# Performance work log

Hardware: AMD Instinct MI355X
Metric: run time of the kernel (lower is better)

Reference implementation:

```python
import jax, jax.numpy as jnp
import numpy as np

B, L, F, P = 128, 256, 4, 4   # dialogs, dialog length, future/past links
IN, H, C = 1024, 256, 7
N = B * L


def _build_edges():
    # same structure as build_intra_graph: self-loop + F future + P past per node
    i = np.arange(L)
    ss, tt = [], []
    for d in range(-P, F + 1):
        j = i + d
        m = (j >= 0) & (j < L)
        ss.append(i[m]); tt.append(j[m])
    s = np.concatenate(ss); t = np.concatenate(tt)
    offs = (np.arange(B) * L)[:, None]
    S = (s[None, :] + offs).ravel()
    T = (t[None, :] + offs).ravel()
    return np.stack([S, T]).astype(np.int32)


def setup_inputs() -> dict:
    key = jax.random.key(0)
    ks = jax.random.split(key, 16)
    ei = _build_edges()
    speakers = np.asarray(jax.random.randint(ks[0], (N,), 0, 2), dtype=np.int32)
    rel = (speakers[ei[0]] * speakers[ei[1]]).astype(np.int32)
    sd_in = 1.0 / np.sqrt(IN)
    sd_h = 1.0 / np.sqrt(H)
    return {
        "input": jax.random.normal(ks[1], (N, IN), jnp.float32),
        "dialog_lengths": jnp.full((B,), L, jnp.int32),
        "speakers": jnp.asarray(speakers),
        "labels": jax.random.randint(ks[2], (N,), 0, C, jnp.int32),
        "edge_index": jnp.asarray(ei),
        "rel_type": jnp.asarray(rel),
        # RGCNConv(IN, H, num_relations=2): per-relation weight, root weight, bias
        "W_rgcn": jax.random.normal(ks[3], (2, IN, H), jnp.float32) * sd_in,
        "W_root": jax.random.normal(ks[4], (IN, H), jnp.float32) * sd_in,
        "b_rgcn": jax.random.normal(ks[5], (H,), jnp.float32) * 0.01,
        # GraphConv(H, H): lin_rel (on aggregated neighbors, with bias), lin_root (no bias)
        "W_rel": jax.random.normal(ks[6], (H, H), jnp.float32) * sd_h,
        "b_rel": jax.random.normal(ks[7], (H,), jnp.float32) * 0.01,
        "W_grt": jax.random.normal(ks[8], (H, H), jnp.float32) * sd_h,
        # skip_con: Linear(IN, H)
        "W_skip": jax.random.normal(ks[9], (IN, H), jnp.float32) * sd_in,
        "b_skip": jax.random.normal(ks[10], (H,), jnp.float32) * 0.01,
        # classify: Linear(H, C)
        "W_cls": jax.random.normal(ks[11], (H, C), jnp.float32) * sd_h,
        "b_cls": jax.random.normal(ks[12], (C,), jnp.float32) * 0.01,
    }


def reference(input, dialog_lengths, speakers, labels, edge_index, rel_type,
              W_rgcn, W_root, b_rgcn, W_rel, b_rel, W_grt,
              W_skip, b_skip, W_cls, b_cls):
    n = input.shape[0]
    src, dst = edge_index[0], edge_index[1]
    seg = jax.ops.segment_sum

    # --- RGCNConv: out_i = x_i @ W_root + b + sum_r mean_{j in N_r(i)} x_j @ W_r
    t = jnp.einsum('ni,rio->rno', input, W_rgcn)      # [2, N, H]
    msg = t[rel_type, src]                            # [E, H] relation-specific messages
    h = input @ W_root + b_rgcn
    for r in range(2):
        m = (rel_type == r).astype(input.dtype)       # [E]
        s = seg(msg * m[:, None], dst, num_segments=n)
        cnt = seg(m, dst, num_segments=n)
        h = h + s / jnp.maximum(cnt, 1.0)[:, None]    # mean aggregation per relation

    # --- GraphConv (aggr='add'): out_i = W_rel @ sum_j h_j + b_rel + W_grt @ h_i
    neigh = seg(h[src], dst, num_segments=n)          # [N, H]
    h2 = neigh @ W_rel + b_rel + h @ W_grt

    # --- skip connection + classifier
    out = (h2 + input @ W_skip + b_skip) @ W_cls + b_cls  # [N, C]

    # --- cross entropy (mean)
    logp = jax.nn.log_softmax(out, axis=-1)
    loss = -jnp.mean(jnp.take_along_axis(logp, labels[:, None].astype(jnp.int32), axis=1))
    return out, loss
```

## Files before the change

kernel.cpp:

```cpp
#include <hip/hip_runtime.h>

#define NN 32768
#define INF 1024
#define HF 256

typedef __bf16 bf16x8 __attribute__((ext_vector_type(8)));
typedef float f32x4 __attribute__((ext_vector_type(4)));

__device__ __forceinline__ float bf2f(unsigned short u) {
  union { unsigned int i; float f; } v; v.i = ((unsigned int)u) << 16; return v.f;
}
__device__ __forceinline__ unsigned short f2bf(float f) {
  union { float f; unsigned int i; } v; v.f = f;
  unsigned int x = v.i;
  return (unsigned short)((x + 0x7fffu + ((x >> 16) & 1u)) >> 16);
}

__device__ __forceinline__ void ld_lds16(const unsigned short* g, unsigned short* l) {
  __builtin_amdgcn_global_load_lds(
      (__attribute__((address_space(1))) const unsigned int*)g,
      (__attribute__((address_space(3))) unsigned int*)l, 16, 0, 0);
}

__global__ __launch_bounds__(256)
void diagcn_prep(const float* __restrict__ x, const float* __restrict__ Wrgcn,
                 const float* __restrict__ Wroot, const float* __restrict__ Wskip,
                 const float* __restrict__ Wgrt, const float* __restrict__ Wrel,
                 unsigned short* __restrict__ Xbf, unsigned short* __restrict__ WbigT,
                 unsigned short* __restrict__ WsmT) {
  int bid = blockIdx.x;
  if (bid < 32768) {
    int idx = bid * 256 + threadIdx.x;
    float4 v = ((const float4*)x)[idx];
    ushort4 u; u.x = f2bf(v.x); u.y = f2bf(v.y); u.z = f2bf(v.z); u.w = f2bf(v.w);
    ((ushort4*)Xbf)[idx] = u;
    return;
  }
  __shared__ float tile[64 * 65];
  int tb = bid - 32768;
  const float* src;
  int k0, ncol0;
  unsigned short* dst;
  int ldd, nrow0;
  if (tb < 256) {
    int tn = tb >> 4, tk = tb & 15;
    int mat = tn >> 2;
    src = (mat == 0) ? Wrgcn : (mat == 1) ? (Wrgcn + 262144) : (mat == 2) ? Wroot : Wskip;
    k0 = tk * 64; ncol0 = (tn & 3) * 64;
    dst = WbigT; ldd = 1024; nrow0 = tn * 64;
  } else {
    int t2 = tb - 256;
    int tn = t2 >> 3, tk = t2 & 7;
    src = (tk < 4) ? Wgrt : Wrel;
    k0 = (tk & 3) * 64; ncol0 = tn * 64;
    dst = WsmT; ldd = 512; nrow0 = tn * 64;
    k0 = k0;
  }
  int kdst0 = (tb < 256) ? k0 : (((tb - 256) & 7) * 64);
  int c = threadIdx.x & 63, rb = threadIdx.x >> 6;
#pragma unroll
  for (int it = 0; it < 16; ++it) {
    int r = rb + it * 4;
    tile[r * 65 + c] = src[(size_t)(k0 + r) * 256 + ncol0 + c];
  }
  __syncthreads();
  int kk = threadIdx.x & 63;
#pragma unroll
  for (int it = 0; it < 16; ++it) {
    int nn = rb + it * 4;
    dst[(size_t)(nrow0 + nn) * ldd + kdst0 + kk] = f2bf(tile[kk * 65 + nn]);
  }
}

template <int EPI, int NT, int L2NT>
__global__ __launch_bounds__(256)
void diagcn_gemm(const unsigned short* __restrict__ A, const unsigned short* __restrict__ BT,
                 void* __restrict__ Cout, const unsigned short* __restrict__ Yfull,
                 const float* __restrict__ brel, const float* __restrict__ bskip, int K) {
  __shared__ unsigned short As[128 * 64];
  __shared__ unsigned short Bs[128 * 64];
  const int tid = threadIdx.x;
  const int w = tid >> 6, lane = tid & 63;
  const int wm = w >> 1, wn = w & 1;
  const int quad = lane >> 4, l15 = lane & 15;
  const int b = blockIdx.x;
  const int m0 = (((b & 7) << 5) + (b >> (3 + L2NT))) << 7;
  const int n0 = ((b >> 3) & (NT - 1)) << 7;
  const int rowg = lane >> 3;
  const int kbsw = (lane & 7) ^ rowg;

  f32x4 acc[4][4] = {};

  const unsigned short* Abase = A + (size_t)m0 * K + kbsw * 8;
  const unsigned short* Bbase = BT + (size_t)n0 * K + kbsw * 8;

  for (int k0 = 0; k0 < K; k0 += 64) {
#pragma unroll
    for (int t = 0; t < 4; ++t) {
      int grp = w * 4 + t;
      int rl = grp * 8 + rowg;
      ld_lds16(Abase + (size_t)rl * K + k0, &As[grp * 512]);
      ld_lds16(Bbase + (size_t)rl * K + k0, &Bs[grp * 512]);
    }
    __syncthreads();
#pragma unroll
    for (int ks = 0; ks < 2; ++ks) {
      bf16x8 av[4], bv[4];
      int kb = ks * 4 + quad;
#pragma unroll
      for (int i = 0; i < 4; ++i) {
        int ra = wm * 64 + i * 16 + l15;
        int rb = wn * 64 + i * 16 + l15;
        av[i] = *(const bf16x8*)&As[ra * 64 + ((kb ^ (ra & 7)) << 3)];
        bv[i] = *(const bf16x8*)&Bs[rb * 64 + ((kb ^ (rb & 7)) << 3)];
      }
#pragma unroll
      for (int i = 0; i < 4; ++i)
#pragma unroll
        for (int j = 0; j < 4; ++j)
          acc[i][j] = __builtin_amdgcn_mfma_f32_16x16x32_bf16(av[i], bv[j], acc[i][j], 0, 0, 0);
    }
    __syncthreads();
  }

  if (EPI == 0) {
    unsigned short* Y = (unsigned short*)Cout;
#pragma unroll
    for (int i = 0; i < 4; ++i)
#pragma unroll
      for (int j = 0; j < 4; ++j) {
        int row = m0 + wm * 64 + i * 16 + quad * 4;
        int col = n0 + wn * 64 + j * 16 + l15;
#pragma unroll
        for (int r = 0; r < 4; ++r)
          Y[(size_t)(row + r) * 1024 + col] = f2bf(acc[i][j][r]);
      }
  } else {
    float* Z = (float*)Cout;
#pragma unroll
    for (int i = 0; i < 4; ++i)
#pragma unroll
      for (int j = 0; j < 4; ++j) {
        int row = m0 + wm * 64 + i * 16 + quad * 4;
        int col = n0 + wn * 64 + j * 16 + l15;
#pragma unroll
        for (int r = 0; r < 4; ++r) {
          float v = acc[i][j][r] + brel[col] + bskip[col] +
                    bf2f(Yfull[(size_t)(row + r) * 1024 + 768 + col]);
          Z[(size_t)(row + r) * 256 + col] = v;
        }
      }
  }
}

__global__ __launch_bounds__(256)
void diagcn_h(const unsigned short* __restrict__ Y, const int* __restrict__ spk,
              const float* __restrict__ brgcn, unsigned short* __restrict__ A2) {
  int b = blockIdx.x;
  int node = ((b & 7) << 12) + ((b >> 3) << 2) + (threadIdx.x >> 6);
  int lane = threadIdx.x & 63, c0 = lane << 2;
  int p = node & 255, dbase = node - p;
  int si = spk[node];
  float a0[4] = {0, 0, 0, 0}, a1[4] = {0, 0, 0, 0};
  float n0 = 0.f, n1 = 0.f;
#pragma unroll
  for (int d = -4; d <= 4; ++d) {
    int pj = p + d;
    float w = (pj >= 0 && pj < 256) ? 1.f : 0.f;
    int jc = pj < 0 ? 0 : (pj > 255 ? 255 : pj);
    int nj = dbase + jc;
    int rel = si & spk[nj];
    ushort4 v = *(const ushort4*)&Y[(size_t)nj * 1024 + (rel << 8) + c0];
    float w1 = rel ? w : 0.f, w0 = rel ? 0.f : w;
    a0[0] += bf2f(v.x) * w0; a1[0] += bf2f(v.x) * w1;
    a0[1] += bf2f(v.y) * w0; a1[1] += bf2f(v.y) * w1;
    a0[2] += bf2f(v.z) * w0; a1[2] += bf2f(v.z) * w1;
    a0[3] += bf2f(v.w) * w0; a1[3] += bf2f(v.w) * w1;
    n0 += w0; n1 += w1;
  }
  ushort4 vr = *(const ushort4*)&Y[(size_t)node * 1024 + 512 + c0];
  float4 bb = *(const float4*)&brgcn[c0];
  float i0 = 1.f / fmaxf(n0, 1.f), i1 = 1.f / fmaxf(n1, 1.f);
  ushort4 u;
  u.x = f2bf(bf2f(vr.x) + bb.x + a0[0] * i0 + a1[0] * i1);
  u.y = f2bf(bf2f(vr.y) + bb.y + a0[1] * i0 + a1[1] * i1);
  u.z = f2bf(bf2f(vr.z) + bb.z + a0[2] * i0 + a1[2] * i1);
  u.w = f2bf(bf2f(vr.w) + bb.w + a0[3] * i0 + a1[3] * i1);
  *(ushort4*)&A2[(size_t)node * 512 + c0] = u;
}

__global__ __launch_bounds__(256)
void diagcn_neigh(unsigned short* __restrict__ A2) {
  int b = blockIdx.x;
  int node = ((b & 7) << 12) + ((b >> 3) << 2) + (threadIdx.x >> 6);
  int lane = threadIdx.x & 63, c0 = lane << 2;
  int p = node & 255, dbase = node - p;
  float s[4] = {0, 0, 0, 0};
#pragma unroll
  for (int d = -4; d <= 4; ++d) {
    int pj = p + d;
    float w = (pj >= 0 && pj < 256) ? 1.f : 0.f;
    int jc = pj < 0 ? 0 : (pj > 255 ? 255 : pj);
    ushort4 v = *(const ushort4*)&A2[(size_t)(dbase + jc) * 512 + c0];
    s[0] += bf2f(v.x) * w; s[1] += bf2f(v.y) * w;
    s[2] += bf2f(v.z) * w; s[3] += bf2f(v.w) * w;
  }
  ushort4 u; u.x = f2bf(s[0]); u.y = f2bf(s[1]); u.z = f2bf(s[2]); u.w = f2bf(s[3]);
  *(ushort4*)&A2[(size_t)node * 512 + 256 + c0] = u;
}

__global__ __launch_bounds__(256)
void diagcn_out(const float* __restrict__ z, const float* __restrict__ Wcls,
                const float* __restrict__ bcls, const int* __restrict__ labels,
                float* __restrict__ out, float* __restrict__ lossp) {
  __shared__ float Wc[256 * 7 + 7];
  for (int i = threadIdx.x; i < 256 * 7 + 7; i += 256)
    Wc[i] = (i < 1792) ? Wcls[i] : bcls[i - 1792];
  __syncthreads();
  int node = blockIdx.x * 4 + (threadIdx.x >> 6);
  int lane = threadIdx.x & 63;
  int c0 = lane << 2;
  float4 zv = *(const float4*)&z[(size_t)node * 256 + c0];
  float zz[4] = {zv.x, zv.y, zv.z, zv.w};
  float pr[7] = {0, 0, 0, 0, 0, 0, 0};
#pragma unroll
  for (int cc = 0; cc < 4; ++cc) {
    const float* wr = &Wc[(c0 + cc) * 7];
#pragma unroll
    for (int k = 0; k < 7; ++k) pr[k] += zz[cc] * wr[k];
  }
#pragma unroll
  for (int o = 32; o > 0; o >>= 1)
#pragma unroll
    for (int k = 0; k < 7; ++k) pr[k] += __shfl_down(pr[k], o, 64);
  if (lane == 0) {
    float o7[7], m = -1e30f;
#pragma unroll
    for (int k = 0; k < 7; ++k) {
      o7[k] = pr[k] + Wc[1792 + k];
      out[(size_t)node * 7 + k] = o7[k];
      m = fmaxf(m, o7[k]);
    }
    float s = 0;
#pragma unroll
    for (int k = 0; k < 7; ++k) s += expf(o7[k] - m);
    int lab = labels[node];
    lossp[node] = m + logf(s) - o7[lab];
  }
}

__global__ void diagcn_lred(const float* __restrict__ lp, float* __restrict__ dst) {
  __shared__ float sm[256];
  float s = 0;
  for (int i = threadIdx.x; i < NN; i += 256) s += lp[i];
  sm[threadIdx.x] = s;
  __syncthreads();
  for (int o = 128; o > 0; o >>= 1) {
    if (threadIdx.x < o) sm[threadIdx.x] += sm[threadIdx.x + o];
    __syncthreads();
  }
  if (threadIdx.x == 0) dst[0] = sm[0] * (1.0f / (float)NN);
}

extern "C" void kernel_launch(void* const* d_in, const int* in_sizes, int n_in,
                              void* d_out, int out_size, void* d_ws, size_t ws_size,
                              hipStream_t stream) {
  const float* x      = (const float*)d_in[0];
  const int* speakers = (const int*)d_in[2];
  const int* labels   = (const int*)d_in[3];
  const float* Wrgcn  = (const float*)d_in[6];
  const float* Wroot  = (const float*)d_in[7];
  const float* brgcn  = (const float*)d_in[8];
  const float* Wrel   = (const float*)d_in[9];
  const float* brel   = (const float*)d_in[10];
  const float* Wgrt   = (const float*)d_in[11];
  const float* Wskip  = (const float*)d_in[12];
  const float* bskip  = (const float*)d_in[13];
  const float* Wcls   = (const float*)d_in[14];
  const float* bcls   = (const float*)d_in[15];
  float* out = (float*)d_out;

  const size_t OFF_XBF  = 0;
  const size_t OFF_WBIG = 67108864;
  const size_t OFF_WSM  = 69206016;
  const size_t OFF_Y    = 69468160;
  const size_t OFF_A2   = 136577024;
  const size_t NEED     = 170131456;
  if (ws_size < NEED) return;

  char* ws = (char*)d_ws;
  unsigned short* Xbf   = (unsigned short*)(ws + OFF_XBF);
  unsigned short* WbigT = (unsigned short*)(ws + OFF_WBIG);
  unsigned short* WsmT  = (unsigned short*)(ws + OFF_WSM);
  unsigned short* Y     = (unsigned short*)(ws + OFF_Y);
  unsigned short* A2    = (unsigned short*)(ws + OFF_A2);
  float* z              = (float*)(ws + OFF_XBF);
  float* lossp          = (float*)(ws + OFF_XBF + 33554432);

  diagcn_prep<<<dim3(32768 + 288), dim3(256), 0, stream>>>(x, Wrgcn, Wroot, Wskip, Wgrt, Wrel,
                                                           Xbf, WbigT, WsmT);
  diagcn_gemm<0, 8, 3><<<dim3(2048), dim3(256), 0, stream>>>(Xbf, WbigT, (void*)Y,
                                                             nullptr, nullptr, nullptr, 1024);
  diagcn_h<<<dim3(NN / 4), dim3(256), 0, stream>>>(Y, speakers, brgcn, A2);
  diagcn_neigh<<<dim3(NN / 4), dim3(256), 0, stream>>>(A2);
  diagcn_gemm<1, 2, 1><<<dim3(512), dim3(256), 0, stream>>>(A2, WsmT, (void*)z,
                                                            Y, brel, bskip, 512);
  diagcn_out<<<dim3(NN / 4), dim3(256), 0, stream>>>(z, Wcls, bcls, labels, out, lossp);
  diagcn_lred<<<dim3(1), dim3(256), 0, stream>>>(lossp, out + (size_t)NN * 7);
}
```

Before: 405.1 us.

## Fuse classifier and loss into second GEMM epilogue, widen gather vectors

The second GEMM now covers all 256 output columns per block (64-row tiles), so each row's full hidden vector is in registers. The epilogue applies the biases, the skip term and the 7-class classifier, then reduces log-softmax cross-entropy via shuffles and atomics into the loss. This removes the fp32 z round-trip and the separate output and loss-reduction kernels. The aggregation kernels also switch to 8-wide bf16 loads, two nodes per wave. Costs are an atomic-order-dependent loss and a larger per-block B tile in LDS.

```diff
diff --git a/kernel.cpp b/kernel.cpp
--- a/kernel.cpp
+++ b/kernel.cpp
@@ -6,6 +6,7 @@
 
 typedef __bf16 bf16x8 __attribute__((ext_vector_type(8)));
 typedef float f32x4 __attribute__((ext_vector_type(4)));
+typedef unsigned short u16x8 __attribute__((ext_vector_type(8)));
 
 __device__ __forceinline__ float bf2f(unsigned short u) {
   union { unsigned int i; float f; } v; v.i = ((unsigned int)u) << 16; return v.f;
@@ -27,9 +28,10 @@
                  const float* __restrict__ Wroot, const float* __restrict__ Wskip,
                  const float* __restrict__ Wgrt, const float* __restrict__ Wrel,
                  unsigned short* __restrict__ Xbf, unsigned short* __restrict__ WbigT,
-                 unsigned short* __restrict__ WsmT) {
+                 unsigned short* __restrict__ WsmT, float* __restrict__ loss) {
   int bid = blockIdx.x;
   if (bid < 32768) {
+    if (bid == 0 && threadIdx.x == 0) loss[0] = 0.f;
     int idx = bid * 256 + threadIdx.x;
     float4 v = ((const float4*)x)[idx];
     ushort4 u; u.x = f2bf(v.x); u.y = f2bf(v.y); u.z = f2bf(v.z); u.w = f2bf(v.w);
@@ -54,7 +56,6 @@
     src = (tk < 4) ? Wgrt : Wrel;
     k0 = (tk & 3) * 64; ncol0 = tn * 64;
     dst = WsmT; ldd = 512; nrow0 = tn * 64;
-    k0 = k0;
   }
   int kdst0 = (tb < 256) ? k0 : (((tb - 256) & 7) * 64);
   int c = threadIdx.x & 63, rb = threadIdx.x >> 6;
@@ -72,11 +73,10 @@
   }
 }
 
-template <int EPI, int NT, int L2NT>
-__global__ __launch_bounds__(256)
-void diagcn_gemm(const unsigned short* __restrict__ A, const unsigned short* __restrict__ BT,
-                 void* __restrict__ Cout, const unsigned short* __restrict__ Yfull,
-                 const float* __restrict__ brel, const float* __restrict__ bskip, int K) {
+__global__ __launch_bounds__(256)
+void diagcn_gemm1(const unsigned short* __restrict__ A, const unsigned short* __restrict__ BT,
+                  unsigned short* __restrict__ Y) {
+  const int K = 1024;
   __shared__ unsigned short As[128 * 64];
   __shared__ unsigned short Bs[128 * 64];
   const int tid = threadIdx.x;
@@ -84,13 +84,12 @@
   const int wm = w >> 1, wn = w & 1;
   const int quad = lane >> 4, l15 = lane & 15;
   const int b = blockIdx.x;
-  const int m0 = (((b & 7) << 5) + (b >> (3 + L2NT))) << 7;
-  const int n0 = ((b >> 3) & (NT - 1)) << 7;
+  const int m0 = (((b & 7) << 5) + (b >> 6)) << 7;
+  const int n0 = ((b >> 3) & 7) << 7;
   const int rowg = lane >> 3;
   const int kbsw = (lane & 7) ^ rowg;
 
   f32x4 acc[4][4] = {};
-
   const unsigned short* Abase = A + (size_t)m0 * K + kbsw * 8;
   const unsigned short* Bbase = BT + (size_t)n0 * K + kbsw * 8;
 
@@ -110,9 +109,9 @@
 #pragma unroll
       for (int i = 0; i < 4; ++i) {
         int ra = wm * 64 + i * 16 + l15;
-        int rb = wn * 64 + i * 16 + l15;
+        int rb2 = wn * 64 + i * 16 + l15;
         av[i] = *(const bf16x8*)&As[ra * 64 + ((kb ^ (ra & 7)) << 3)];
-        bv[i] = *(const bf16x8*)&Bs[rb * 64 + ((kb ^ (rb & 7)) << 3)];
+        bv[i] = *(const bf16x8*)&Bs[rb2 * 64 + ((kb ^ (rb2 & 7)) << 3)];
       }
 #pragma unroll
       for (int i = 0; i < 4; ++i)
@@ -122,46 +121,28 @@
     }
     __syncthreads();
   }
-
-  if (EPI == 0) {
-    unsigned short* Y = (unsigned short*)Cout;
-#pragma unroll
-    for (int i = 0; i < 4; ++i)
-#pragma unroll
-      for (int j = 0; j < 4; ++j) {
-        int row = m0 + wm * 64 + i * 16 + quad * 4;
-        int col = n0 + wn * 64 + j * 16 + l15;
-#pragma unroll
-        for (int r = 0; r < 4; ++r)
-          Y[(size_t)(row + r) * 1024 + col] = f2bf(acc[i][j][r]);
-      }
-  } else {
-    float* Z = (float*)Cout;
-#pragma unroll
-    for (int i = 0; i < 4; ++i)
-#pragma unroll
-      for (int j = 0; j < 4; ++j) {
-        int row = m0 + wm * 64 + i * 16 + quad * 4;
-        int col = n0 + wn * 64 + j * 16 + l15;
-#pragma unroll
-        for (int r = 0; r < 4; ++r) {
-          float v = acc[i][j][r] + brel[col] + bskip[col] +
-                    bf2f(Yfull[(size_t)(row + r) * 1024 + 768 + col]);
-          Z[(size_t)(row + r) * 256 + col] = v;
-        }
-      }
-  }
+#pragma unroll
+  for (int i = 0; i < 4; ++i)
+#pragma unroll
+    for (int j = 0; j < 4; ++j) {
+      int row = m0 + wm * 64 + i * 16 + quad * 4;
+      int col = n0 + wn * 64 + j * 16 + l15;
+#pragma unroll
+      for (int r = 0; r < 4; ++r)
+        Y[(size_t)(row + r) * 1024 + col] = f2bf(acc[i][j][r]);
+    }
 }
 
 __global__ __launch_bounds__(256)
 void diagcn_h(const unsigned short* __restrict__ Y, const int* __restrict__ spk,
               const float* __restrict__ brgcn, unsigned short* __restrict__ A2) {
   int b = blockIdx.x;
-  int node = ((b & 7) << 12) + ((b >> 3) << 2) + (threadIdx.x >> 6);
-  int lane = threadIdx.x & 63, c0 = lane << 2;
+  int wv = threadIdx.x >> 6, lane = threadIdx.x & 63;
+  int half = lane >> 5, li = lane & 31, c0 = li << 3;
+  int node = ((b & 7) << 12) + ((b >> 3) << 3) + wv * 2 + half;
   int p = node & 255, dbase = node - p;
   int si = spk[node];
-  float a0[4] = {0, 0, 0, 0}, a1[4] = {0, 0, 0, 0};
+  float a0[8] = {}, a1[8] = {};
   float n0 = 0.f, n1 = 0.f;
 #pragma unroll
   for (int d = -4; d <= 4; ++d) {
@@ -170,96 +151,145 @@
     int jc = pj < 0 ? 0 : (pj > 255 ? 255 : pj);
     int nj = dbase + jc;
     int rel = si & spk[nj];
-    ushort4 v = *(const ushort4*)&Y[(size_t)nj * 1024 + (rel << 8) + c0];
+    u16x8 v = *(const u16x8*)&Y[(size_t)nj * 1024 + (rel << 8) + c0];
     float w1 = rel ? w : 0.f, w0 = rel ? 0.f : w;
-    a0[0] += bf2f(v.x) * w0; a1[0] += bf2f(v.x) * w1;
-    a0[1] += bf2f(v.y) * w0; a1[1] += bf2f(v.y) * w1;
-    a0[2] += bf2f(v.z) * w0; a1[2] += bf2f(v.z) * w1;
-    a0[3] += bf2f(v.w) * w0; a1[3] += bf2f(v.w) * w1;
+#pragma unroll
+    for (int k = 0; k < 8; ++k) {
+      float f = bf2f(v[k]);
+      a0[k] += f * w0; a1[k] += f * w1;
+    }
     n0 += w0; n1 += w1;
   }
-  ushort4 vr = *(const ushort4*)&Y[(size_t)node * 1024 + 512 + c0];
-  float4 bb = *(const float4*)&brgcn[c0];
+  u16x8 vr = *(const u16x8*)&Y[(size_t)node * 1024 + 512 + c0];
   float i0 = 1.f / fmaxf(n0, 1.f), i1 = 1.f / fmaxf(n1, 1.f);
-  ushort4 u;
-  u.x = f2bf(bf2f(vr.x) + bb.x + a0[0] * i0 + a1[0] * i1);
-  u.y = f2bf(bf2f(vr.y) + bb.y + a0[1] * i0 + a1[1] * i1);
-  u.z = f2bf(bf2f(vr.z) + bb.z + a0[2] * i0 + a1[2] * i1);
-  u.w = f2bf(bf2f(vr.w) + bb.w + a0[3] * i0 + a1[3] * i1);
-  *(ushort4*)&A2[(size_t)node * 512 + c0] = u;
+  u16x8 u;
+#pragma unroll
+  for (int k = 0; k < 8; ++k)
+    u[k] = f2bf(bf2f(vr[k]) + brgcn[c0 + k] + a0[k] * i0 + a1[k] * i1);
+  *(u16x8*)&A2[(size_t)node * 512 + c0] = u;
 }
 
 __global__ __launch_bounds__(256)
 void diagcn_neigh(unsigned short* __restrict__ A2) {
   int b = blockIdx.x;
-  int node = ((b & 7) << 12) + ((b >> 3) << 2) + (threadIdx.x >> 6);
-  int lane = threadIdx.x & 63, c0 = lane << 2;
+  int wv = threadIdx.x >> 6, lane = threadIdx.x & 63;
+  int half = lane >> 5, li = lane & 31, c0 = li << 3;
+  int node = ((b & 7) << 12) + ((b >> 3) << 3) + wv * 2 + half;
   int p = node & 255, dbase = node - p;
-  float s[4] = {0, 0, 0, 0};
+  float s[8] = {};
 #pragma unroll
   for (int d = -4; d <= 4; ++d) {
     int pj = p + d;
     float w = (pj >= 0 && pj < 256) ? 1.f : 0.f;
     int jc = pj < 0 ? 0 : (pj > 255 ? 255 : pj);
-    ushort4 v = *(const ushort4*)&A2[(size_t)(dbase + jc) * 512 + c0];
-    s[0] += bf2f(v.x) * w; s[1] += bf2f(v.y) * w;
-    s[2] += bf2f(v.z) * w; s[3] += bf2f(v.w) * w;
-  }
-  ushort4 u; u.x = f2bf(s[0]); u.y = f2bf(s[1]); u.z = f2bf(s[2]); u.w = f2bf(s[3]);
-  *(ushort4*)&A2[(size_t)node * 512 + 256 + c0] = u;
-}
-
-__global__ __launch_bounds__(256)
-void diagcn_out(const float* __restrict__ z, const float* __restrict__ Wcls,
-                const float* __restrict__ bcls, const int* __restrict__ labels,
-                float* __restrict__ out, float* __restrict__ lossp) {
-  __shared__ float Wc[256 * 7 + 7];
-  for (int i = threadIdx.x; i < 256 * 7 + 7; i += 256)
-    Wc[i] = (i < 1792) ? Wcls[i] : bcls[i - 1792];
-  __syncthreads();
-  int node = blockIdx.x * 4 + (threadIdx.x >> 6);
-  int lane = threadIdx.x & 63;
-  int c0 = lane << 2;
-  float4 zv = *(const float4*)&z[(size_t)node * 256 + c0];
-  float zz[4] = {zv.x, zv.y, zv.z, zv.w};
-  float pr[7] = {0, 0, 0, 0, 0, 0, 0};
-#pragma unroll
-  for (int cc = 0; cc < 4; ++cc) {
-    const float* wr = &Wc[(c0 + cc) * 7];
-#pragma unroll
-    for (int k = 0; k < 7; ++k) pr[k] += zz[cc] * wr[k];
-  }
-#pragma unroll
-  for (int o = 32; o > 0; o >>= 1)
-#pragma unroll
-    for (int k = 0; k < 7; ++k) pr[k] += __shfl_down(pr[k], o, 64);
-  if (lane == 0) {
-    float o7[7], m = -1e30f;
-#pragma unroll
-    for (int k = 0; k < 7; ++k) {
-      o7[k] = pr[k] + Wc[1792 + k];
-      out[(size_t)node * 7 + k] = o7[k];
-      m = fmaxf(m, o7[k]);
-    }
-    float s = 0;
-#pragma unroll
-    for (int k = 0; k < 7; ++k) s += expf(o7[k] - m);
-    int lab = labels[node];
-    lossp[node] = m + logf(s) - o7[lab];
-  }
-}
-
-__global__ void diagcn_lred(const float* __restrict__ lp, float* __restrict__ dst) {
-  __shared__ float sm[256];
-  float s = 0;
-  for (int i = threadIdx.x; i < NN; i += 256) s += lp[i];
-  sm[threadIdx.x] = s;
-  __syncthreads();
-  for (int o = 128; o > 0; o >>= 1) {
-    if (threadIdx.x < o) sm[threadIdx.x] += sm[threadIdx.x + o];
+    u16x8 v = *(const u16x8*)&A2[(size_t)(dbase + jc) * 512 + c0];
+#pragma unroll
+    for (int k = 0; k < 8; ++k) s[k] += bf2f(v[k]) * w;
+  }
+  u16x8 u;
+#pragma unroll
+  for (int k = 0; k < 8; ++k) u[k] = f2bf(s[k]);
+  *(u16x8*)&A2[(size_t)node * 512 + 256 + c0] = u;
+}
+
+__global__ __launch_bounds__(256)
+void diagcn_gemm2(const unsigned short* __restrict__ A, const unsigned short* __restrict__ BT,
+                  const unsigned short* __restrict__ Y, const float* __restrict__ Wcls,
+                  const float* __restrict__ bcls, const float* __restrict__ brel,
+                  const float* __restrict__ bskip, const int* __restrict__ labels,
+                  float* __restrict__ out, float* __restrict__ loss) {
+  const int K = 512;
+  __shared__ unsigned short As[64 * 64];
+  __shared__ unsigned short Bs[256 * 64];
+  __shared__ float Wc[2312];
+  for (int i = threadIdx.x; i < 2312; i += 256) {
+    float v;
+    if (i < 1792) v = Wcls[i];
+    else if (i < 1799) v = bcls[i - 1792];
+    else if (i < 1800) v = 0.f;
+    else if (i < 2056) v = brel[i - 1800];
+    else v = bskip[i - 2056];
+    Wc[i] = v;
+  }
+  const int tid = threadIdx.x;
+  const int w = tid >> 6, lane = tid & 63;
+  const int quad = lane >> 4, l15 = lane & 15;
+  const int b = blockIdx.x;
+  const int m0 = (((b & 7) << 6) + (b >> 3)) << 6;
+  const int rowg = lane >> 3;
+  const int kbsw = (lane & 7) ^ rowg;
+
+  f32x4 acc[16] = {};
+  const unsigned short* Abase = A + (size_t)m0 * K + kbsw * 8;
+  const unsigned short* Bbase = BT + kbsw * 8;
+
+  for (int k0 = 0; k0 < K; k0 += 64) {
+#pragma unroll
+    for (int t = 0; t < 2; ++t) {
+      int grp = w * 2 + t;
+      ld_lds16(Abase + (size_t)(grp * 8 + rowg) * K + k0, &As[grp * 512]);
+    }
+#pragma unroll
+    for (int t = 0; t < 8; ++t) {
+      int grp = w * 8 + t;
+      ld_lds16(Bbase + (size_t)(grp * 8 + rowg) * K + k0, &Bs[grp * 512]);
+    }
     __syncthreads();
-  }
-  if (threadIdx.x == 0) dst[0] = sm[0] * (1.0f / (float)NN);
+#pragma unroll
+    for (int ks = 0; ks < 2; ++ks) {
+      int kb = ks * 4 + quad;
+      int ra = w * 16 + l15;
+      bf16x8 av = *(const bf16x8*)&As[ra * 64 + ((kb ^ (ra & 7)) << 3)];
+#pragma unroll
+      for (int j = 0; j < 16; ++j) {
+        int rb2 = j * 16 + l15;
+        bf16x8 bv = *(const bf16x8*)&Bs[rb2 * 64 + ((kb ^ (rb2 & 7)) << 3)];
+        acc[j] = __builtin_amdgcn_mfma_f32_16x16x32_bf16(av, bv, acc[j], 0, 0, 0);
+      }
+    }
+    __syncthreads();
+  }
+
+  float wsum[4][7] = {};
+#pragma unroll
+  for (int j = 0; j < 16; ++j) {
+    int col = j * 16 + l15;
+    float bb = Wc[1800 + col] + Wc[2056 + col];
+#pragma unroll
+    for (int r = 0; r < 4; ++r) {
+      int row = m0 + w * 16 + quad * 4 + r;
+      float z = acc[j][r] + bb + bf2f(Y[(size_t)row * 1024 + 768 + col]);
+#pragma unroll
+      for (int c = 0; c < 7; ++c) wsum[r][c] += z * Wc[col * 7 + c];
+    }
+  }
+#pragma unroll
+  for (int o = 1; o < 16; o <<= 1)
+#pragma unroll
+    for (int r = 0; r < 4; ++r)
+#pragma unroll
+      for (int c = 0; c < 7; ++c) wsum[r][c] += __shfl_xor(wsum[r][c], o, 64);
+
+  float lsum = 0.f;
+#pragma unroll
+  for (int r = 0; r < 4; ++r) {
+    int row = m0 + w * 16 + quad * 4 + r;
+    float o7[7], mx = -1e30f;
+#pragma unroll
+    for (int c = 0; c < 7; ++c) {
+      o7[c] = wsum[r][c] + Wc[1792 + c];
+      mx = fmaxf(mx, o7[c]);
+    }
+    if (l15 < 7) out[(size_t)row * 7 + l15] = o7[l15];
+    float s = 0.f;
+#pragma unroll
+    for (int c = 0; c < 7; ++c) s += expf(o7[c] - mx);
+    int lab = labels[row];
+    lsum += mx + logf(s) - o7[lab];
+  }
+  lsum += __shfl_xor(lsum, 16, 64);
+  lsum += __shfl_xor(lsum, 32, 64);
+  if (lane == 0) atomicAdd(loss, lsum * (1.0f / (float)NN));
 }
 
 extern "C" void kernel_launch(void* const* d_in, const int* in_sizes, int n_in,
@@ -279,6 +309,7 @@
   const float* Wcls   = (const float*)d_in[14];
   const float* bcls   = (const float*)d_in[15];
   float* out = (float*)d_out;
+  float* loss = out + (size_t)NN * 7;
 
   const size_t OFF_XBF  = 0;
   const size_t OFF_WBIG = 67108864;
@@ -294,17 +325,12 @@
   unsigned short* WsmT  = (unsigned short*)(ws + OFF_WSM);
   unsigned short* Y     = (unsigned short*)(ws + OFF_Y);
   unsigned short* A2    = (unsigned short*)(ws + OFF_A2);
-  float* z              = (float*)(ws + OFF_XBF);
-  float* lossp          = (float*)(ws + OFF_XBF + 33554432);
-
-  diagcn_prep<<<dim3(32768 + 288), dim3(256), 0, stream>>>(x, Wrgcn, Wroot, Wskip, Wgrt, Wrel,
-                                                           Xbf, WbigT, WsmT);
-  diagcn_gemm<0, 8, 3><<<dim3(2048), dim3(256), 0, stream>>>(Xbf, WbigT, (void*)Y,
-                                                             nullptr, nullptr, nullptr, 1024);
-  diagcn_h<<<dim3(NN / 4), dim3(256), 0, stream>>>(Y, speakers, brgcn, A2);
-  diagcn_neigh<<<dim3(NN / 4), dim3(256), 0, stream>>>(A2);
-  diagcn_gemm<1, 2, 1><<<dim3(512), dim3(256), 0, stream>>>(A2, WsmT, (void*)z,
-                                                            Y, brel, bskip, 512);
-  diagcn_out<<<dim3(NN / 4), dim3(256), 0, stream>>>(z, Wcls, bcls, labels, out, lossp);
-  diagcn_lred<<<dim3(1), dim3(256), 0, stream>>>(lossp, out + (size_t)NN * 7);
-}
+
+  diagcn_prep<<<dim3(33056), dim3(256), 0, stream>>>(x, Wrgcn, Wroot, Wskip, Wgrt, Wrel,
+                                                     Xbf, WbigT, WsmT, loss);
+  diagcn_gemm1<<<dim3(2048), dim3(256), 0, stream>>>(Xbf, WbigT, Y);
+  diagcn_h<<<dim3(NN / 8), dim3(256), 0, stream>>>(Y, speakers, brgcn, A2);
+  diagcn_neigh<<<dim3(NN / 8), dim3(256), 0, stream>>>(A2);
+  diagcn_gemm2<<<dim3(512), dim3(256), 0, stream>>>(A2, WsmT, Y, Wcls, bcls, brel, bskip,
+                                                    labels, out, loss);
+}
```

Measured after the change: 381.2 us. 1.06x faster.
